# Performance work log

Hardware: AMD Instinct MI355X
Metric: run time of the kernel (lower is better)

Reference implementation:

```python
import jax, jax.numpy as jnp
import numpy as np

V, E, H, G, L, T, B = 32000, 1024, 16, 4, 8, 1024, 2
NKV = H // G          # kv heads = 4
D = E // H            # head dim = 64
BLOCK = 1024          # block_size
EPS = 1e-5


def setup_inputs() -> dict:
    key = jax.random.key(0)
    ks = jax.random.split(key, 12)
    f32 = jnp.float32
    return {
        "idx": jax.random.randint(ks[0], (B, T), 0, V),
        "tok_emb": jax.random.normal(ks[1], (V, E), f32),
        "pos_emb": jax.random.normal(ks[2], (BLOCK, E), f32),
        "q_proj": jax.random.normal(ks[3], (L, E, G, NKV, D), f32) / E**0.5,
        "kv_proj": jax.random.normal(ks[4], (L, 2, E, NKV, D), f32) / E**0.5,
        "out_proj": jax.random.normal(ks[5], (L, E, E), f32) / (D * H)**0.5,
        "fc_in": jax.random.normal(ks[6], (L, E, 4 * E), f32) / E**0.5,
        "fc_out": jax.random.normal(ks[7], (L, 4 * E, E), f32) / (4 * E)**0.5,
        "scale": jnp.ones((L, 2, E), f32),
        "out_scale": jnp.ones((E,), f32),
        "lm_head": jax.random.normal(ks[8], (E, V), f32) / E**0.5,
    }


def _ln(x, w):
    mu = jnp.mean(x, axis=-1, keepdims=True)
    var = jnp.var(x, axis=-1, keepdims=True)
    return (x - mu) * jax.lax.rsqrt(var + EPS) * w


def reference(idx, tok_emb, pos_emb, q_proj, kv_proj, out_proj, fc_in, fc_out, scale, out_scale, lm_head):
    x = tok_emb[idx] + pos_emb[:T]                         # [B,T,E]
    causal = jnp.tril(jnp.ones((T, T), bool))              # [T,T]
    neg_inf = jnp.float32(-jnp.inf)

    def layer(x, params):
        w_kv, w_q, w_out, fc1, fc2, lscale = params
        h = _ln(x, lscale[0])                              # pre-LN (note: residual uses h, matching source)
        q = jnp.einsum('btc,cgnd->bgntd', h, w_q)          # [B,G,NKV,T,D]
        kv = jnp.einsum('btc,scnd->sbntd', h, w_kv)        # [2,B,NKV,T,D]
        k, v = kv[0], kv[1]
        att = jnp.einsum('bgnqd,bnkd->bgnqk', q, k) * (D ** -0.5)
        att = jnp.where(causal, att, neg_inf)
        att = jax.nn.softmax(att, axis=-1)
        o = jnp.einsum('bgnqk,bnkd->bgnqd', att, v)        # [B,G,NKV,T,D]
        o = jnp.transpose(o, (0, 3, 1, 2, 4)).reshape(B, T, E)
        o = jnp.einsum('btc,cd->btd', o, w_out)
        h = h + o
        h = _ln(h, lscale[1])
        mlp = jax.nn.relu(jnp.einsum('btc,cf->btf', h, fc1))
        mlp = jnp.einsum('btf,fc->btc', mlp, fc2)
        return h + mlp, None

    x, _ = jax.lax.scan(layer, x, (kv_proj, q_proj, out_proj, fc_in, fc_out, scale))
    x = _ln(x, out_scale)
    logits = jnp.einsum('btc,cv->btv', x, lm_head)         # [B,T,V]
    return logits
```

## Files before the change

kernel.cpp:

```cpp
#include <hip/hip_runtime.h>
#include <hip/hip_bf16.h>

typedef __attribute__((ext_vector_type(8))) short bf16x8;
typedef __attribute__((ext_vector_type(4))) short bf16x4;
typedef __attribute__((ext_vector_type(4))) float f32x4;

#define LB __launch_bounds__(256)

__device__ __forceinline__ unsigned short f2b(float f) {
  __hip_bfloat16 h = __float2bfloat16(f);
  return __builtin_bit_cast(unsigned short, h);
}

#define GLDS(gp, lp)                                                        \
  __builtin_amdgcn_global_load_lds(                                         \
      (const __attribute__((address_space(1))) void*)(gp),                  \
      (__attribute__((address_space(3))) void*)(lp), 16, 0, 0)

__global__ LB void embed_kernel(const int* __restrict__ idx, const float* __restrict__ tok,
                                const float* __restrict__ pos, float* __restrict__ X) {
  const int m = blockIdx.x;
  const int t = m & 1023;
  const int token = idx[m];
  const int c = threadIdx.x * 4;
  const float4 a = *(const float4*)(tok + (size_t)token * 1024 + c);
  const float4 p = *(const float4*)(pos + (size_t)t * 1024 + c);
  float4 o; o.x = a.x + p.x; o.y = a.y + p.y; o.z = a.z + p.z; o.w = a.w + p.w;
  *(float4*)(X + (size_t)m * 1024 + c) = o;
}

template<bool WF32, bool ADD3>
__global__ LB void ln_kernel(const float* __restrict__ X, const float* __restrict__ A1,
                             const float* __restrict__ A2, const float* __restrict__ W,
                             float* __restrict__ Yf, unsigned short* __restrict__ Yb) {
  const int row = blockIdx.x;
  const int c = threadIdx.x * 4;
  const size_t base = (size_t)row * 1024 + c;
  float4 v = *(const float4*)(X + base);
  if (ADD3) {
    const float4 a1 = *(const float4*)(A1 + base);
    const float4 a2 = *(const float4*)(A2 + base);
    v.x += a1.x + a2.x; v.y += a1.y + a2.y; v.z += a1.z + a2.z; v.w += a1.w + a2.w;
  }
  float s = v.x + v.y + v.z + v.w;
  float q = v.x*v.x + v.y*v.y + v.z*v.z + v.w*v.w;
  #pragma unroll
  for (int d = 32; d > 0; d >>= 1) { s += __shfl_down(s, d); q += __shfl_down(q, d); }
  __shared__ float ss[4], sq[4];
  const int wid = threadIdx.x >> 6;
  if ((threadIdx.x & 63) == 0) { ss[wid] = s; sq[wid] = q; }
  __syncthreads();
  const float fs = ss[0] + ss[1] + ss[2] + ss[3];
  const float fq = sq[0] + sq[1] + sq[2] + sq[3];
  const float mean = fs * (1.0f / 1024.0f);
  const float var = fq * (1.0f / 1024.0f) - mean * mean;
  const float rstd = rsqrtf(var + 1e-5f);
  const float4 w = *(const float4*)(W + c);
  float4 o;
  o.x = (v.x - mean) * rstd * w.x; o.y = (v.y - mean) * rstd * w.y;
  o.z = (v.z - mean) * rstd * w.z; o.w = (v.w - mean) * rstd * w.w;
  if (WF32) *(float4*)(Yf + base) = o;
  unsigned long long pk = (unsigned long long)f2b(o.x)
      | ((unsigned long long)f2b(o.y) << 16)
      | ((unsigned long long)f2b(o.z) << 32)
      | ((unsigned long long)f2b(o.w) << 48);
  *(unsigned long long*)(Yb + base) = pk;
}

__global__ LB void transpose_w(const float* __restrict__ src, unsigned short* __restrict__ dst,
                               int C, int rowOff, int ldDst) {
  __shared__ float tile[32][33];
  const int c0 = blockIdx.x * 32, r0 = blockIdx.y * 32;
  const int tx = threadIdx.x & 31, ty = threadIdx.x >> 5;
  #pragma unroll
  for (int u = 0; u < 4; ++u)
    tile[ty + u * 8][tx] = src[(size_t)(r0 + ty + u * 8) * C + c0 + tx];
  __syncthreads();
  const int ci = threadIdx.x >> 4;
  const int rp = threadIdx.x & 15;
  #pragma unroll
  for (int u = 0; u < 2; ++u) {
    const int c = ci + u * 16;
    unsigned int pk = (unsigned int)f2b(tile[rp * 2][c])
                    | ((unsigned int)f2b(tile[rp * 2 + 1][c]) << 16);
    *(unsigned int*)&dst[(size_t)(rowOff + c0 + c) * ldDst + r0 + rp * 2] = pk;
  }
}

__global__ LB void transpose_v(const unsigned short* __restrict__ src, unsigned short* __restrict__ dst) {
  __shared__ unsigned short tile[32][33];
  const int b = blockIdx.z;
  const int c0 = blockIdx.x * 32, t0 = blockIdx.y * 32;
  const int tx = threadIdx.x & 31, ty = threadIdx.x >> 5;
  #pragma unroll
  for (int u = 0; u < 4; ++u)
    tile[ty + u * 8][tx] = src[(size_t)(b * 1024 + t0 + ty + u * 8) * 1536 + 1280 + c0 + tx];
  __syncthreads();
  #pragma unroll
  for (int u = 0; u < 4; ++u)
    dst[((size_t)b * 256 + c0 + ty + u * 8) * 1024 + t0 + tx] = tile[tx][ty + u * 8];
}

__global__ LB void attn_fused(const unsigned short* __restrict__ qkvb,
                              const unsigned short* __restrict__ vT,
                              unsigned short* __restrict__ ob) {
  const int qt = 15 - blockIdx.x, bh = blockIdx.y;
  const int b = bh >> 4, hh = bh & 15, n = hh & 3;
  const int tid = threadIdx.x, lane = tid & 63, w = tid >> 6;
  const int g = lane >> 4, c = lane & 15;
  const int q0w = qt * 64 + w * 16;
  const int qrow = q0w + c;

  __shared__ unsigned short lsP[4][16 * 64];
  unsigned short* Pw = lsP[w];

  const unsigned short* Qb = qkvb + (size_t)(b * 1024 + q0w) * 1536 + hh * 64;
  const unsigned short* Kb = qkvb + (size_t)(b * 1024) * 1536 + 1024 + n * 64;
  const unsigned short* Vb = vT + (size_t)((b * 4 + n) * 64) * 1024;

  bf16x8 qf[2];
  #pragma unroll
  for (int ks = 0; ks < 2; ++ks)
    qf[ks] = *(const bf16x8*)(Qb + (size_t)c * 1536 + ks * 32 + g * 8);

  f32x4 accO[4] = {};
  float mr = -1e30f, lr = 0.0f;

  for (int kt = 0; kt <= qt; ++kt) {
    const int kb = kt * 64;
    f32x4 st[4] = {};
    #pragma unroll
    for (int ks = 0; ks < 2; ++ks) {
      bf16x8 kf[4];
      #pragma unroll
      for (int mi = 0; mi < 4; ++mi)
        kf[mi] = *(const bf16x8*)(Kb + (size_t)(kb + mi * 16 + c) * 1536 + ks * 32 + g * 8);
      #pragma unroll
      for (int mi = 0; mi < 4; ++mi)
        st[mi] = __builtin_amdgcn_mfma_f32_16x16x32_bf16(kf[mi], qf[ks], st[mi], 0, 0, 0);
    }
    const bool dg = (kt == qt);
    float mx = mr;
    #pragma unroll
    for (int mi = 0; mi < 4; ++mi)
      #pragma unroll
      for (int j = 0; j < 4; ++j) {
        float v = st[mi][j] * 0.125f;
        if (dg && (kb + mi * 16 + g * 4 + j) > qrow) v = -1e30f;
        st[mi][j] = v;
        mx = fmaxf(mx, v);
      }
    mx = fmaxf(mx, __shfl_xor(mx, 16));
    mx = fmaxf(mx, __shfl_xor(mx, 32));
    const float al = __expf(mr - mx);
    float sum = 0.0f;
    #pragma unroll
    for (int mi = 0; mi < 4; ++mi) {
      bf16x4 pk;
      #pragma unroll
      for (int j = 0; j < 4; ++j) {
        const float e = __expf(st[mi][j] - mx);
        sum += e;
        pk[j] = (short)f2b(e);
      }
      *(bf16x4*)&Pw[c * 64 + ((mi * 16 + g * 4) ^ ((c & 7) << 3))] = pk;
    }
    sum += __shfl_xor(sum, 16);
    sum += __shfl_xor(sum, 32);
    lr = lr * al + sum;
    mr = mx;
    float aj[4];
    #pragma unroll
    for (int j = 0; j < 4; ++j) aj[j] = __shfl(al, g * 4 + j);
    #pragma unroll
    for (int dj = 0; dj < 4; ++dj)
      #pragma unroll
      for (int j = 0; j < 4; ++j) accO[dj][j] *= aj[j];
    #pragma unroll
    for (int ks = 0; ks < 2; ++ks) {
      const int col = (((ks * 4 + g) ^ (c & 7)) << 3);
      const bf16x8 pa = *(const bf16x8*)&Pw[c * 64 + col];
      bf16x8 vf[4];
      #pragma unroll
      for (int dj = 0; dj < 4; ++dj)
        vf[dj] = *(const bf16x8*)(Vb + (size_t)(dj * 16 + c) * 1024 + kb + ks * 32 + g * 8);
      #pragma unroll
      for (int dj = 0; dj < 4; ++dj)
        accO[dj] = __builtin_amdgcn_mfma_f32_16x16x32_bf16(pa, vf[dj], accO[dj], 0, 0, 0);
    }
  }

  const float linv = 1.0f / lr;
  float lj[4];
  #pragma unroll
  for (int j = 0; j < 4; ++j) lj[j] = __shfl(linv, g * 4 + j);
  unsigned short* obase = ob + (size_t)(b * 1024 + q0w) * 1024 + hh * 64;
  #pragma unroll
  for (int dj = 0; dj < 4; ++dj)
    #pragma unroll
    for (int j = 0; j < 4; ++j)
      obase[(size_t)(g * 4 + j) * 1024 + dj * 16 + c] = f2b(accO[dj][j] * lj[j]);
}

template<int BM, int BN, bool BF16OUT, bool RELU, bool RESID>
__global__ LB void gemm_nt(const unsigned short* __restrict__ A, const unsigned short* __restrict__ Bt,
                           void* __restrict__ Cv, const float* __restrict__ Res,
                           int K, int lda, int ldb, int ldc, long long sC) {
  constexpr int BK = 64;
  constexpr int WM = BM / 2, WN = BN / 2;
  constexpr int FM = WM / 16, FN = WN / 16;
  constexpr int PA = BM / 32, PB = BN / 32;
  int f = blockIdx.x + gridDim.x * blockIdx.y;
  const int nwg = gridDim.x * gridDim.y;
  if ((nwg & 7) == 0) f = (f & 7) * (nwg >> 3) + (f >> 3);
  const int bx = f % gridDim.x, by = f / gridDim.x;
  const long long coff = (long long)blockIdx.z * sC;
  const unsigned short* Az = A + (size_t)blockIdx.z * K;
  const unsigned short* Bz = Bt + (size_t)blockIdx.z * K;

  const int tid = threadIdx.x;
  const int lane = tid & 63, wid = tid >> 6;
  const int wr = wid >> 1, wc = wid & 1;
  const int m0 = bx * BM, n0 = by * BN;

  __shared__ unsigned short lsA[BM * BK];
  __shared__ unsigned short lsB[BN * BK];

  f32x4 acc[FM][FN] = {};

  const int srow = tid >> 3;
  const int scol = ((tid & 7) ^ (srow & 7)) << 3;
  const unsigned short* gA = Az + (size_t)(m0 + srow) * lda + scol;
  const unsigned short* gB = Bz + (size_t)(n0 + srow) * ldb + scol;
  unsigned short* lA = lsA + tid * 8;
  unsigned short* lB = lsB + tid * 8;

  const int fr = lane & 15;
  const int j7 = lane & 7;
  const int g4 = lane >> 4;

  for (int k0 = 0; k0 < K; k0 += BK) {
    if (k0) __syncthreads();
    #pragma unroll
    for (int p = 0; p < PA; ++p)
      GLDS(gA + (size_t)(p * 32) * lda + k0, lA + p * 2048);
    #pragma unroll
    for (int p = 0; p < PB; ++p)
      GLDS(gB + (size_t)(p * 32) * ldb + k0, lB + p * 2048);
    __syncthreads();

    #pragma unroll
    for (int ks = 0; ks < 2; ++ks) {
      const int col = (((ks * 4 + g4) ^ j7) << 3);
      bf16x8 af[FM], bfv[FN];
      #pragma unroll
      for (int mi = 0; mi < FM; ++mi)
        af[mi] = *(const bf16x8*)&lsA[(wr * WM + mi * 16 + fr) * BK + col];
      #pragma unroll
      for (int nj = 0; nj < FN; ++nj)
        bfv[nj] = *(const bf16x8*)&lsB[(wc * WN + nj * 16 + fr) * BK + col];
      #pragma unroll
      for (int mi = 0; mi < FM; ++mi)
        #pragma unroll
        for (int nj = 0; nj < FN; ++nj)
          acc[mi][nj] = __builtin_amdgcn_mfma_f32_16x16x32_bf16(af[mi], bfv[nj], acc[mi][nj], 0, 0, 0);
    }
  }

  const int r0 = (lane >> 4) * 4, c0 = lane & 15;
  #pragma unroll
  for (int mi = 0; mi < FM; ++mi) {
    #pragma unroll
    for (int nj = 0; nj < FN; ++nj) {
      const int c = n0 + wc * WN + nj * 16 + c0;
      #pragma unroll
      for (int j = 0; j < 4; ++j) {
        const int r = m0 + wr * WM + mi * 16 + r0 + j;
        float v = acc[mi][nj][j];
        if (RELU) v = fmaxf(v, 0.0f);
        if (RESID) v += Res[(size_t)r * ldc + c];
        const size_t o = (size_t)(coff + (long long)r * ldc + c);
        if (BF16OUT) ((unsigned short*)Cv)[o] = f2b(v);
        else ((float*)Cv)[o] = v;
      }
    }
  }
}

extern "C" void kernel_launch(void* const* d_in, const int* in_sizes, int n_in,
                              void* d_out, int out_size, void* d_ws, size_t ws_size,
                              hipStream_t stream) {
  (void)in_sizes; (void)n_in; (void)out_size;
  const int*   idx      = (const int*)d_in[0];
  const float* tok_emb  = (const float*)d_in[1];
  const float* pos_emb  = (const float*)d_in[2];
  const float* q_proj   = (const float*)d_in[3];
  const float* kv_proj  = (const float*)d_in[4];
  const float* out_proj = (const float*)d_in[5];
  const float* fc_in    = (const float*)d_in[6];
  const float* fc_out   = (const float*)d_in[7];
  const float* scale    = (const float*)d_in[8];
  const float* out_scl  = (const float*)d_in[9];
  const float* lm_head  = (const float*)d_in[10];
  float* out = (float*)d_out;

  char* ws = (char*)d_ws;
  size_t off = 0;
  auto alloc = [&](size_t bytes) -> void* {
    void* p = ws + off;
    off += (bytes + 255) & ~(size_t)255;
    return p;
  };
  unsigned short* WqkvT = (unsigned short*)alloc((size_t)1536 * 1024 * 2);
  unsigned short* WoT   = (unsigned short*)alloc((size_t)1024 * 1024 * 2);
  unsigned short* F1T   = (unsigned short*)alloc((size_t)4096 * 1024 * 2);
  unsigned short* F2T   = (unsigned short*)alloc((size_t)1024 * 4096 * 2);
  float*  xbuf  = (float*)alloc((size_t)2048 * 1024 * 4);
  float*  hbuf  = (float*)alloc((size_t)2048 * 1024 * 4);
  float*  h2buf = (float*)alloc((size_t)2048 * 1024 * 4);
  unsigned short* actb  = (unsigned short*)alloc((size_t)2048 * 1024 * 2);
  unsigned short* qkvb  = (unsigned short*)alloc((size_t)2048 * 1536 * 2);
  unsigned short* vT    = (unsigned short*)alloc((size_t)2 * 256 * 1024 * 2);
  unsigned short* LmT   = (unsigned short*)alloc((size_t)32000 * 1024 * 2);
  unsigned short* ob    = (unsigned short*)alloc((size_t)2048 * 1024 * 2);
  unsigned short* m1    = (unsigned short*)alloc((size_t)2048 * 4096 * 2);
  if (off > ws_size) return;
  float* p0 = (float*)LmT;
  float* p1 = p0 + (size_t)2048 * 1024;

  const dim3 thr(256);

  embed_kernel<<<dim3(2048), thr, 0, stream>>>(idx, tok_emb, pos_emb, xbuf);

  for (int l = 0; l < 8; ++l) {
    transpose_w<<<dim3(32, 32), thr, 0, stream>>>(q_proj + (size_t)l * 1024 * 1024, WqkvT, 1024, 0, 1024);
    transpose_w<<<dim3(8, 32), thr, 0, stream>>>(kv_proj + (size_t)l * 2 * 1024 * 256, WqkvT, 256, 1024, 1024);
    transpose_w<<<dim3(8, 32), thr, 0, stream>>>(kv_proj + (size_t)l * 2 * 1024 * 256 + 1024 * 256, WqkvT, 256, 1280, 1024);
    transpose_w<<<dim3(32, 32), thr, 0, stream>>>(out_proj + (size_t)l * 1024 * 1024, WoT, 1024, 0, 1024);
    transpose_w<<<dim3(128, 32), thr, 0, stream>>>(fc_in + (size_t)l * 1024 * 4096, F1T, 4096, 0, 1024);
    transpose_w<<<dim3(32, 128), thr, 0, stream>>>(fc_out + (size_t)l * 4096 * 1024, F2T, 1024, 0, 4096);

    const float* w1 = scale + (size_t)l * 2048;
    const float* w2 = w1 + 1024;

    if (l == 0)
      ln_kernel<true, false><<<dim3(2048), thr, 0, stream>>>(xbuf, nullptr, nullptr, w1, hbuf, actb);
    else
      ln_kernel<true, true><<<dim3(2048), thr, 0, stream>>>(h2buf, p0, p1, w1, hbuf, actb);
    gemm_nt<128, 64, true, false, false><<<dim3(16, 24), thr, 0, stream>>>(
        actb, WqkvT, qkvb, nullptr, 1024, 1024, 1024, 1536, 0);
    transpose_v<<<dim3(8, 32, 2), thr, 0, stream>>>(qkvb, vT);
    attn_fused<<<dim3(16, 32), thr, 0, stream>>>(qkvb, vT, ob);
    gemm_nt<128, 64, false, false, true><<<dim3(16, 16), thr, 0, stream>>>(
        ob, WoT, xbuf, hbuf, 1024, 1024, 1024, 1024, 0);
    ln_kernel<true, false><<<dim3(2048), thr, 0, stream>>>(xbuf, nullptr, nullptr, w2, h2buf, actb);
    gemm_nt<128, 128, true, true, false><<<dim3(16, 32), thr, 0, stream>>>(
        actb, F1T, m1, nullptr, 1024, 1024, 1024, 4096, 0);
    gemm_nt<128, 128, false, false, false><<<dim3(16, 8, 2), thr, 0, stream>>>(
        m1, F2T, p0, nullptr, 2048, 4096, 4096, 1024, 2048LL * 1024);
  }

  ln_kernel<false, true><<<dim3(2048), thr, 0, stream>>>(h2buf, p0, p1, out_scl, nullptr, actb);
  transpose_w<<<dim3(1000, 32), thr, 0, stream>>>(lm_head, LmT, 32000, 0, 1024);
  gemm_nt<128, 128, false, false, false><<<dim3(16, 250), thr, 0, stream>>>(
      actb, LmT, out, nullptr, 1024, 1024, 1024, 32000, 0);
}
```

Measured before the change: 1.799 ms.

## Fuse V transpose into QKV GEMM, drop split-K FC2, merge weight transposes

The QKV GEMM epilogue now also writes the V columns transposed into vT, so the separate transpose_v launch goes away. FC2 is no longer split-K into two partial buffers summed by the next LayerNorm. It becomes a single 128x64 GEMM with a fused residual add into xbuf, which simplifies the LN kernel. The q/out and k/v weight transposes are merged into z-indexed launches, and s_setprio brackets the MFMA groups in attention. In exchange, FC2 gets a single K=4096 pass with fewer workgroups, and the GEMM epilogue does extra scattered 8-byte stores.

Measured after the change: 1.908 ms. +6.0%, slower.

```diff
diff --git a/kernel.cpp b/kernel.cpp
--- a/kernel.cpp
+++ b/kernel.cpp
@@ -29,19 +29,13 @@
   *(float4*)(X + (size_t)m * 1024 + c) = o;
 }
 
-template<bool WF32, bool ADD3>
-__global__ LB void ln_kernel(const float* __restrict__ X, const float* __restrict__ A1,
-                             const float* __restrict__ A2, const float* __restrict__ W,
+template<bool WF32>
+__global__ LB void ln_kernel(const float* __restrict__ X, const float* __restrict__ W,
                              float* __restrict__ Yf, unsigned short* __restrict__ Yb) {
   const int row = blockIdx.x;
   const int c = threadIdx.x * 4;
   const size_t base = (size_t)row * 1024 + c;
-  float4 v = *(const float4*)(X + base);
-  if (ADD3) {
-    const float4 a1 = *(const float4*)(A1 + base);
-    const float4 a2 = *(const float4*)(A2 + base);
-    v.x += a1.x + a2.x; v.y += a1.y + a2.y; v.z += a1.z + a2.z; v.w += a1.w + a2.w;
-  }
+  const float4 v = *(const float4*)(X + base);
   float s = v.x + v.y + v.z + v.w;
   float q = v.x*v.x + v.y*v.y + v.z*v.z + v.w*v.w;
   #pragma unroll
@@ -87,18 +81,27 @@
   }
 }
 
-__global__ LB void transpose_v(const unsigned short* __restrict__ src, unsigned short* __restrict__ dst) {
-  __shared__ unsigned short tile[32][33];
-  const int b = blockIdx.z;
-  const int c0 = blockIdx.x * 32, t0 = blockIdx.y * 32;
+__global__ LB void transpose_w2(const float* __restrict__ s0, const float* __restrict__ s1,
+                                unsigned short* __restrict__ dst, int C,
+                                int rowOff0, int rowOffZ, int ldDst) {
+  __shared__ float tile[32][33];
+  const float* src = blockIdx.z ? s1 : s0;
+  const int rowOff = rowOff0 + (int)blockIdx.z * rowOffZ;
+  const int c0 = blockIdx.x * 32, r0 = blockIdx.y * 32;
   const int tx = threadIdx.x & 31, ty = threadIdx.x >> 5;
   #pragma unroll
   for (int u = 0; u < 4; ++u)
-    tile[ty + u * 8][tx] = src[(size_t)(b * 1024 + t0 + ty + u * 8) * 1536 + 1280 + c0 + tx];
+    tile[ty + u * 8][tx] = src[(size_t)(r0 + ty + u * 8) * C + c0 + tx];
   __syncthreads();
-  #pragma unroll
-  for (int u = 0; u < 4; ++u)
-    dst[((size_t)b * 256 + c0 + ty + u * 8) * 1024 + t0 + tx] = tile[tx][ty + u * 8];
+  const int ci = threadIdx.x >> 4;
+  const int rp = threadIdx.x & 15;
+  #pragma unroll
+  for (int u = 0; u < 2; ++u) {
+    const int c = ci + u * 16;
+    unsigned int pk = (unsigned int)f2b(tile[rp * 2][c])
+                    | ((unsigned int)f2b(tile[rp * 2 + 1][c]) << 16);
+    *(unsigned int*)&dst[(size_t)(rowOff + c0 + c) * ldDst + r0 + rp * 2] = pk;
+  }
 }
 
 __global__ LB void attn_fused(const unsigned short* __restrict__ qkvb,
@@ -135,9 +138,11 @@
       #pragma unroll
       for (int mi = 0; mi < 4; ++mi)
         kf[mi] = *(const bf16x8*)(Kb + (size_t)(kb + mi * 16 + c) * 1536 + ks * 32 + g * 8);
+      __builtin_amdgcn_s_setprio(1);
       #pragma unroll
       for (int mi = 0; mi < 4; ++mi)
         st[mi] = __builtin_amdgcn_mfma_f32_16x16x32_bf16(kf[mi], qf[ks], st[mi], 0, 0, 0);
+      __builtin_amdgcn_s_setprio(0);
     }
     const bool dg = (kt == qt);
     float mx = mr;
@@ -184,9 +189,11 @@
       #pragma unroll
       for (int dj = 0; dj < 4; ++dj)
         vf[dj] = *(const bf16x8*)(Vb + (size_t)(dj * 16 + c) * 1024 + kb + ks * 32 + g * 8);
+      __builtin_amdgcn_s_setprio(1);
       #pragma unroll
       for (int dj = 0; dj < 4; ++dj)
         accO[dj] = __builtin_amdgcn_mfma_f32_16x16x32_bf16(pa, vf[dj], accO[dj], 0, 0, 0);
+      __builtin_amdgcn_s_setprio(0);
     }
   }
 
@@ -202,10 +209,11 @@
       obase[(size_t)(g * 4 + j) * 1024 + dj * 16 + c] = f2b(accO[dj][j] * lj[j]);
 }
 
-template<int BM, int BN, bool BF16OUT, bool RELU, bool RESID>
+template<int BM, int BN, bool BF16OUT, bool RELU, bool RESID, bool WVT>
 __global__ LB void gemm_nt(const unsigned short* __restrict__ A, const unsigned short* __restrict__ Bt,
                            void* __restrict__ Cv, const float* __restrict__ Res,
-                           int K, int lda, int ldb, int ldc, long long sC) {
+                           unsigned short* __restrict__ vTo,
+                           int K, int lda, int ldb, int ldc) {
   constexpr int BK = 64;
   constexpr int WM = BM / 2, WN = BN / 2;
   constexpr int FM = WM / 16, FN = WN / 16;
@@ -214,9 +222,6 @@
   const int nwg = gridDim.x * gridDim.y;
   if ((nwg & 7) == 0) f = (f & 7) * (nwg >> 3) + (f >> 3);
   const int bx = f % gridDim.x, by = f / gridDim.x;
-  const long long coff = (long long)blockIdx.z * sC;
-  const unsigned short* Az = A + (size_t)blockIdx.z * K;
-  const unsigned short* Bz = Bt + (size_t)blockIdx.z * K;
 
   const int tid = threadIdx.x;
   const int lane = tid & 63, wid = tid >> 6;
@@ -230,8 +235,8 @@
 
   const int srow = tid >> 3;
   const int scol = ((tid & 7) ^ (srow & 7)) << 3;
-  const unsigned short* gA = Az + (size_t)(m0 + srow) * lda + scol;
-  const unsigned short* gB = Bz + (size_t)(n0 + srow) * ldb + scol;
+  const unsigned short* gA = A + (size_t)(m0 + srow) * lda + scol;
+  const unsigned short* gB = Bt + (size_t)(n0 + srow) * ldb + scol;
   unsigned short* lA = lsA + tid * 8;
   unsigned short* lB = lsB + tid * 8;
 
@@ -273,15 +278,24 @@
     #pragma unroll
     for (int nj = 0; nj < FN; ++nj) {
       const int c = n0 + wc * WN + nj * 16 + c0;
+      const int rb = m0 + wr * WM + mi * 16 + r0;
+      unsigned short us[4];
       #pragma unroll
       for (int j = 0; j < 4; ++j) {
-        const int r = m0 + wr * WM + mi * 16 + r0 + j;
+        const int r = rb + j;
         float v = acc[mi][nj][j];
         if (RELU) v = fmaxf(v, 0.0f);
         if (RESID) v += Res[(size_t)r * ldc + c];
-        const size_t o = (size_t)(coff + (long long)r * ldc + c);
-        if (BF16OUT) ((unsigned short*)Cv)[o] = f2b(v);
+        const size_t o = (size_t)r * ldc + c;
+        if (BF16OUT) { us[j] = f2b(v); ((unsigned short*)Cv)[o] = us[j]; }
         else ((float*)Cv)[o] = v;
+      }
+      if (WVT && c >= 1280) {
+        const int bb = rb >> 10, t0 = rb & 1023;
+        bf16x4 pk;
+        #pragma unroll
+        for (int j = 0; j < 4; ++j) pk[j] = (short)us[j];
+        *(bf16x4*)&vTo[((size_t)(bb * 256 + (c - 1280))) * 1024 + t0] = pk;
       }
     }
   }
@@ -311,8 +325,8 @@
     off += (bytes + 255) & ~(size_t)255;
     return p;
   };
-  unsigned short* WqkvT = (unsigned short*)alloc((size_t)1536 * 1024 * 2);
-  unsigned short* WoT   = (unsigned short*)alloc((size_t)1024 * 1024 * 2);
+  unsigned short* WqkvT = (unsigned short*)alloc((size_t)2560 * 1024 * 2);
+  unsigned short* WoT   = WqkvT + (size_t)1536 * 1024;
   unsigned short* F1T   = (unsigned short*)alloc((size_t)4096 * 1024 * 2);
   unsigned short* F2T   = (unsigned short*)alloc((size_t)1024 * 4096 * 2);
   float*  xbuf  = (float*)alloc((size_t)2048 * 1024 * 4);
@@ -325,43 +339,38 @@
   unsigned short* ob    = (unsigned short*)alloc((size_t)2048 * 1024 * 2);
   unsigned short* m1    = (unsigned short*)alloc((size_t)2048 * 4096 * 2);
   if (off > ws_size) return;
-  float* p0 = (float*)LmT;
-  float* p1 = p0 + (size_t)2048 * 1024;
 
   const dim3 thr(256);
 
   embed_kernel<<<dim3(2048), thr, 0, stream>>>(idx, tok_emb, pos_emb, xbuf);
 
   for (int l = 0; l < 8; ++l) {
-    transpose_w<<<dim3(32, 32), thr, 0, stream>>>(q_proj + (size_t)l * 1024 * 1024, WqkvT, 1024, 0, 1024);
-    transpose_w<<<dim3(8, 32), thr, 0, stream>>>(kv_proj + (size_t)l * 2 * 1024 * 256, WqkvT, 256, 1024, 1024);
-    transpose_w<<<dim3(8, 32), thr, 0, stream>>>(kv_proj + (size_t)l * 2 * 1024 * 256 + 1024 * 256, WqkvT, 256, 1280, 1024);
-    transpose_w<<<dim3(32, 32), thr, 0, stream>>>(out_proj + (size_t)l * 1024 * 1024, WoT, 1024, 0, 1024);
+    const float* qp = q_proj + (size_t)l * 1024 * 1024;
+    const float* op = out_proj + (size_t)l * 1024 * 1024;
+    const float* kvp = kv_proj + (size_t)l * 2 * 1024 * 256;
+    transpose_w2<<<dim3(32, 32, 2), thr, 0, stream>>>(qp, op, WqkvT, 1024, 0, 1536, 1024);
+    transpose_w2<<<dim3(8, 32, 2), thr, 0, stream>>>(kvp, kvp + 1024 * 256, WqkvT, 256, 1024, 256, 1024);
     transpose_w<<<dim3(128, 32), thr, 0, stream>>>(fc_in + (size_t)l * 1024 * 4096, F1T, 4096, 0, 1024);
     transpose_w<<<dim3(32, 128), thr, 0, stream>>>(fc_out + (size_t)l * 4096 * 1024, F2T, 1024, 0, 4096);
 
     const float* w1 = scale + (size_t)l * 2048;
     const float* w2 = w1 + 1024;
 
-    if (l == 0)
-      ln_kernel<true, false><<<dim3(2048), thr, 0, stream>>>(xbuf, nullptr, nullptr, w1, hbuf, actb);
-    else
-      ln_kernel<true, true><<<dim3(2048), thr, 0, stream>>>(h2buf, p0, p1, w1, hbuf, actb);
-    gemm_nt<128, 64, true, false, false><<<dim3(16, 24), thr, 0, stream>>>(
-        actb, WqkvT, qkvb, nullptr, 1024, 1024, 1024, 1536, 0);
-    transpose_v<<<dim3(8, 32, 2), thr, 0, stream>>>(qkvb, vT);
+    ln_kernel<true><<<dim3(2048), thr, 0, stream>>>(xbuf, w1, hbuf, actb);
+    gemm_nt<128, 64, true, false, false, true><<<dim3(16, 24), thr, 0, stream>>>(
+        actb, WqkvT, qkvb, nullptr, vT, 1024, 1024, 1024, 1536);
     attn_fused<<<dim3(16, 32), thr, 0, stream>>>(qkvb, vT, ob);
-    gemm_nt<128, 64, false, false, true><<<dim3(16, 16), thr, 0, stream>>>(
-        ob, WoT, xbuf, hbuf, 1024, 1024, 1024, 1024, 0);
-    ln_kernel<true, false><<<dim3(2048), thr, 0, stream>>>(xbuf, nullptr, nullptr, w2, h2buf, actb);
-    gemm_nt<128, 128, true, true, false><<<dim3(16, 32), thr, 0, stream>>>(
-        actb, F1T, m1, nullptr, 1024, 1024, 1024, 4096, 0);
-    gemm_nt<128, 128, false, false, false><<<dim3(16, 8, 2), thr, 0, stream>>>(
-        m1, F2T, p0, nullptr, 2048, 4096, 4096, 1024, 2048LL * 1024);
-  }
-
-  ln_kernel<false, true><<<dim3(2048), thr, 0, stream>>>(h2buf, p0, p1, out_scl, nullptr, actb);
+    gemm_nt<128, 64, false, false, true, false><<<dim3(16, 16), thr, 0, stream>>>(
+        ob, WoT, xbuf, hbuf, nullptr, 1024, 1024, 1024, 1024);
+    ln_kernel<true><<<dim3(2048), thr, 0, stream>>>(xbuf, w2, h2buf, actb);
+    gemm_nt<128, 128, true, true, false, false><<<dim3(16, 32), thr, 0, stream>>>(
+        actb, F1T, m1, nullptr, nullptr, 1024, 1024, 1024, 4096);
+    gemm_nt<128, 64, false, false, true, false><<<dim3(16, 16), thr, 0, stream>>>(
+        m1, F2T, xbuf, h2buf, nullptr, 4096, 4096, 4096, 1024);
+  }
+
   transpose_w<<<dim3(1000, 32), thr, 0, stream>>>(lm_head, LmT, 32000, 0, 1024);
-  gemm_nt<128, 128, false, false, false><<<dim3(16, 250), thr, 0, stream>>>(
-      actb, LmT, out, nullptr, 1024, 1024, 1024, 32000, 0);
-}
+  ln_kernel<false><<<dim3(2048), thr, 0, stream>>>(xbuf, out_scl, nullptr, actb);
+  gemm_nt<128, 128, false, false, false, false><<<dim3(16, 250), thr, 0, stream>>>(
+      actb, LmT, out, nullptr, nullptr, 1024, 1024, 1024, 32000);
+}
```
